# Performance work log

Measured on AMD Instinct MI355X. Metric: run time of the kernel, lower is better.

## Reference

```python
import jax, jax.numpy as jnp
import numpy as np

NUM_BINS = 32
SIGMA_RATIO = 0.5          # Gaussian Parzen window width relative to bin spacing
SMOOTH_NR = 1e-07
SMOOTH_DR = 1e-07


def setup_inputs() -> dict:
    key = jax.random.key(0)
    k1, k2 = jax.random.split(key)
    shape = (2, 1, 96, 96, 96)
    pred = jax.random.uniform(k1, shape, dtype=jnp.float32)
    target = jax.random.uniform(k2, shape, dtype=jnp.float32)
    return {"pred": pred, "target": target}


def _parzen_weights(img_flat, bin_centers, preterm):
    # img_flat: [B, N]; bin_centers: [nb]
    # Gaussian Parzen window, normalized so each voxel's weights sum to 1 over bins.
    d = img_flat[..., None] - bin_centers          # [B, N, nb]
    w = jnp.exp(-preterm * d * d)                  # [B, N, nb]
    return w / jnp.sum(w, axis=-1, keepdims=True)


def reference(pred, target):
    B = pred.shape[0]
    nb = NUM_BINS
    bin_centers = jnp.linspace(0.0, 1.0, nb, dtype=jnp.float32)  # [nb]
    bin_width = 1.0 / (nb - 1)
    sigma = SIGMA_RATIO * bin_width
    preterm = jnp.float32(1.0 / (2.0 * sigma * sigma))

    p = pred.reshape(B, -1)    # [B, N]
    t = target.reshape(B, -1)  # [B, N]
    N = p.shape[1]

    wa = _parzen_weights(p, bin_centers, preterm)  # [B, N, nb]
    wb = _parzen_weights(t, bin_centers, preterm)  # [B, N, nb]

    # joint histogram [B, nb, nb] and marginals [B, 1, nb]
    pab = jnp.einsum('bni,bnj->bij', wa, wb) / N
    pa = jnp.mean(wa, axis=1, keepdims=True).transpose(0, 2, 1).transpose(0, 2, 1)  # [B,1,nb]
    pa = jnp.mean(wa, axis=1)[:, None, :]  # [B, 1, nb]
    pb = jnp.mean(wb, axis=1)[:, None, :]  # [B, 1, nb]

    # papb = bmm(pa^T, pb): outer product of marginals -> [B, nb, nb]
    papb = jnp.einsum('bki,bkj->bij', pa, pb)

    mi = jnp.sum(pab * jnp.log((pab + SMOOTH_NR) / (papb + SMOOTH_DR) + SMOOTH_DR),
                 axis=(-1, -2))  # [B]
    return -jnp.mean(mi)
```

## Files before the change

kernel.cpp:

```cpp
#include <hip/hip_runtime.h>
#include <hip/hip_bf16.h>

#define NBINS 32
#define LDS_STRIDE 264
#define NTHREADS 256
#define NVOX 884736
#define NSLABS 3456
#define BPB 512
#define NSLOTS 16
#define TILE_HALVES (NBINS * LDS_STRIDE)

typedef __attribute__((ext_vector_type(8))) _Float16 half8;
typedef __attribute__((ext_vector_type(16))) float f32x16;
typedef __attribute__((ext_vector_type(4))) int i32x4;

__device__ __forceinline__ void scatter_rewrite(_Float16* __restrict__ L, int tid, float x,
                                                int& ki_old, bool zero_old) {
    float tt = x * 31.0f;
    float kf = rintf(tt);
    int ki = (int)kf;
    float u = tt - kf;
    if (zero_old) {
#pragma unroll
        for (int o = 0; o < 7; ++o) {
            int b = ki_old + o - 3;
            if (b >= 0 && b < NBINS) L[b * LDS_STRIDE + tid] = (_Float16)0.0f;
        }
    }
    float w[7];
    float s = 0.0f;
#pragma unroll
    for (int o = 0; o < 7; ++o) {
        float d = u - (float)(o - 3);
        float e = __expf(-2.0f * d * d);
        int b = ki + o - 3;
        bool valid = (b >= 0) && (b < NBINS);
        e = valid ? e : 0.0f;
        w[o] = e;
        s += e;
    }
    float rinv = 1.0f / s;
#pragma unroll
    for (int o = 0; o < 7; ++o) {
        int b = ki + o - 3;
        if (b >= 0 && b < NBINS)
            L[b * LDS_STRIDE + tid] = (_Float16)(w[o] * rinv);
    }
    ki_old = ki;
}

__global__ __launch_bounds__(NTHREADS, 4)
void mi_hist_kernel(const float* __restrict__ pred, const float* __restrict__ targ,
                    float* __restrict__ hist ) {
    __shared__ __attribute__((aligned(16))) _Float16 smem[2 * TILE_HALVES];
    _Float16* LA = smem;
    _Float16* LB = smem + TILE_HALVES;

    const int tid = threadIdx.x;
    const int bx = blockIdx.x;
    const int batch = blockIdx.y;
    const float* p = pred + (size_t)batch * NVOX;
    const float* t = targ + (size_t)batch * NVOX;

    const int wid = tid >> 6;
    const int lane = tid & 63;
    const int frag_off = (lane & 31) * LDS_STRIDE + wid * 64 + 8 * (lane >> 5);

    const int nchunks = (bx < 384) ? 7 : 6;

    f32x16 acc;
#pragma unroll
    for (int r = 0; r < 16; ++r) acc[r] = 0.0f;

    {
        i32x4 z = {0, 0, 0, 0};
        i32x4* zp = (i32x4*)smem;
        for (int i = tid; i < (2 * TILE_HALVES) / 8; i += NTHREADS) zp[i] = z;
    }
    float pv = p[(size_t)bx * 256 + tid];
    float tv = t[(size_t)bx * 256 + tid];
    int kiA = 0, kiB = 0;
    __syncthreads();

    for (int c = 0; c < nchunks; ++c) {
        float pn = 0.0f, tn = 0.0f;
        if (c + 1 < nchunks) {
            size_t v = ((size_t)(c + 1) * BPB + bx) * 256 + tid;
            pn = p[v];
            tn = t[v];
        }
        scatter_rewrite(LA, tid, pv, kiA, c > 0);
        scatter_rewrite(LB, tid, tv, kiB, c > 0);
        __syncthreads();

#pragma unroll
        for (int kb = 0; kb < 4; ++kb) {
            half8 af = *(const half8*)&LA[frag_off + kb * 16];
            half8 bf = *(const half8*)&LB[frag_off + kb * 16];
            acc = __builtin_amdgcn_mfma_f32_32x32x16_f16(af, bf, acc, 0, 0, 0);
        }
        __syncthreads();
        pv = pn; tv = tn;
    }

    float* red = (float*)smem;
    const int col = lane & 31;
    const int rlo = 4 * (lane >> 5);
#pragma unroll
    for (int r = 0; r < 16; ++r) {
        int rowc = (r & 3) + 8 * (r >> 2) + rlo;
        red[wid * 1024 + rowc * 32 + col] = acc[r];
    }
    __syncthreads();
    float* H = hist + ((size_t)(bx & (NSLOTS - 1)) * 2 + batch) * 1024;
    for (int idx = tid; idx < 1024; idx += NTHREADS) {
        float s = red[idx] + red[1024 + idx] + red[2048 + idx] + red[3072 + idx];
        atomicAdd(&H[idx], s);
    }
}

__global__ void mi_reduce_kernel(const float* __restrict__ hist, float* __restrict__ out) {
    __shared__ float s_pab[2 * NBINS * NBINS];
    __shared__ double s_pa[2][NBINS];
    __shared__ double s_pb[2][NBINS];
    __shared__ double s_red[256];
    const int tid = threadIdx.x;
    const double invN = 1.0 / (double)NVOX;

    for (int g = tid; g < 512; g += 256) {
        float4 s = make_float4(0.f, 0.f, 0.f, 0.f);
        for (int sl = 0; sl < NSLOTS; ++sl) {
            float4 v = ((const float4*)hist)[sl * 512 + g];
            s.x += v.x; s.y += v.y; s.z += v.z; s.w += v.w;
        }
        ((float4*)s_pab)[g] = s;
    }
    __syncthreads();

    if (tid < 64) {
        int b = tid >> 5, i = tid & 31;
        double s = 0.0;
        for (int j = 0; j < NBINS; ++j) s += (double)s_pab[(b * NBINS + i) * NBINS + j];
        s_pa[b][i] = s * invN;
    } else if (tid < 128) {
        int t2 = tid - 64;
        int b = t2 >> 5, j = t2 & 31;
        double s = 0.0;
        for (int i = 0; i < NBINS; ++i) s += (double)s_pab[(b * NBINS + i) * NBINS + j];
        s_pb[b][j] = s * invN;
    }
    __syncthreads();

    double acc = 0.0;
    for (int idx = tid; idx < 2 * NBINS * NBINS; idx += 256) {
        int b = idx >> 10;
        int cell = idx & 1023;
        int i = cell >> 5, j = cell & 31;
        double pab = (double)s_pab[idx] * invN;
        double papb = s_pa[b][i] * s_pb[b][j];
        acc += pab * log((pab + 1e-7) / (papb + 1e-7) + 1e-7);
    }
    s_red[tid] = acc;
    __syncthreads();
    for (int s2 = 128; s2 > 0; s2 >>= 1) {
        if (tid < s2) s_red[tid] += s_red[tid + s2];
        __syncthreads();
    }
    if (tid == 0) out[0] = (float)(-0.5 * s_red[0]);
}

extern "C" void kernel_launch(void* const* d_in, const int* in_sizes, int n_in,
                              void* d_out, int out_size, void* d_ws, size_t ws_size,
                              hipStream_t stream) {
    const float* pred = (const float*)d_in[0];
    const float* targ = (const float*)d_in[1];
    float* hist = (float*)d_ws;
    float* out = (float*)d_out;

    hipMemsetAsync(hist, 0, NSLOTS * 2 * NBINS * NBINS * sizeof(float), stream);
    dim3 grid(BPB, 2);
    hipLaunchKernelGGL(mi_hist_kernel, grid, dim3(NTHREADS), 0, stream, pred, targ, hist);
    hipLaunchKernelGGL(mi_reduce_kernel, dim3(1), dim3(256), 0, stream, hist, out);
}
```

Measured before the change: 33.73 us.

## Double-buffer LDS weight tiles, trim Parzen window to six bins, resize blocks

Allocates two LDS tile pairs and alternates between them, so one barrier per chunk replaces two and scattering the next chunk can overlap the MFMA reads of the previous one. The Parzen window is cut from 7 to 6 bins by picking the start bin from the sign of the fractional offset, which saves one exp and one LDS store per voxel per image. Blocks go to 192 threads (3 waves), 384 blocks per batch and a uniform 12 chunks, with launch bounds lowered to 2, so work per block is balanced. The cost is twice the LDS per block and possibly lower occupancy. Dropping the far tail bin slightly changes the normalised weights.

```diff
diff --git a/kernel.cpp b/kernel.cpp
--- a/kernel.cpp
+++ b/kernel.cpp
@@ -2,11 +2,11 @@
 #include <hip/hip_bf16.h>
 
 #define NBINS 32
-#define LDS_STRIDE 264
-#define NTHREADS 256
+#define LDS_STRIDE 200
+#define NTHREADS 192
 #define NVOX 884736
-#define NSLABS 3456
-#define BPB 512
+#define BPB 384
+#define NCHUNKS 12
 #define NSLOTS 16
 #define TILE_HALVES (NBINS * LDS_STRIDE)
 
@@ -15,25 +15,26 @@
 typedef __attribute__((ext_vector_type(4))) int i32x4;
 
 __device__ __forceinline__ void scatter_rewrite(_Float16* __restrict__ L, int tid, float x,
-                                                int& ki_old, bool zero_old) {
+                                                int& kb_old, bool zero_old) {
     float tt = x * 31.0f;
     float kf = rintf(tt);
     int ki = (int)kf;
     float u = tt - kf;
+    int kb = ki - 3 + (u > 0.0f ? 1 : 0);
     if (zero_old) {
 #pragma unroll
-        for (int o = 0; o < 7; ++o) {
-            int b = ki_old + o - 3;
+        for (int o = 0; o < 6; ++o) {
+            int b = kb_old + o;
             if (b >= 0 && b < NBINS) L[b * LDS_STRIDE + tid] = (_Float16)0.0f;
         }
     }
-    float w[7];
+    float w[6];
     float s = 0.0f;
 #pragma unroll
-    for (int o = 0; o < 7; ++o) {
-        float d = u - (float)(o - 3);
+    for (int o = 0; o < 6; ++o) {
+        int b = kb + o;
+        float d = tt - (float)b;
         float e = __expf(-2.0f * d * d);
-        int b = ki + o - 3;
         bool valid = (b >= 0) && (b < NBINS);
         e = valid ? e : 0.0f;
         w[o] = e;
@@ -41,20 +42,33 @@
     }
     float rinv = 1.0f / s;
 #pragma unroll
-    for (int o = 0; o < 7; ++o) {
-        int b = ki + o - 3;
+    for (int o = 0; o < 6; ++o) {
+        int b = kb + o;
         if (b >= 0 && b < NBINS)
             L[b * LDS_STRIDE + tid] = (_Float16)(w[o] * rinv);
     }
-    ki_old = ki;
-}
-
-__global__ __launch_bounds__(NTHREADS, 4)
+    kb_old = kb;
+}
+
+__device__ __forceinline__ void do_mfma(const _Float16* __restrict__ bufA,
+                                        const _Float16* __restrict__ bufB,
+                                        int frag_off, f32x16& acc) {
+#pragma unroll
+    for (int kb = 0; kb < 4; ++kb) {
+        half8 af = *(const half8*)&bufA[frag_off + kb * 16];
+        half8 bf = *(const half8*)&bufB[frag_off + kb * 16];
+        acc = __builtin_amdgcn_mfma_f32_32x32x16_f16(af, bf, acc, 0, 0, 0);
+    }
+}
+
+__global__ __launch_bounds__(NTHREADS, 2)
 void mi_hist_kernel(const float* __restrict__ pred, const float* __restrict__ targ,
                     float* __restrict__ hist ) {
-    __shared__ __attribute__((aligned(16))) _Float16 smem[2 * TILE_HALVES];
-    _Float16* LA = smem;
-    _Float16* LB = smem + TILE_HALVES;
+    __shared__ __attribute__((aligned(16))) _Float16 smem[4 * TILE_HALVES];
+    _Float16* A0 = smem;
+    _Float16* B0 = smem + TILE_HALVES;
+    _Float16* A1 = smem + 2 * TILE_HALVES;
+    _Float16* B1 = smem + 3 * TILE_HALVES;
 
     const int tid = threadIdx.x;
     const int bx = blockIdx.x;
@@ -66,8 +80,6 @@
     const int lane = tid & 63;
     const int frag_off = (lane & 31) * LDS_STRIDE + wid * 64 + 8 * (lane >> 5);
 
-    const int nchunks = (bx < 384) ? 7 : 6;
-
     f32x16 acc;
 #pragma unroll
     for (int r = 0; r < 16; ++r) acc[r] = 0.0f;
@@ -75,33 +87,43 @@
     {
         i32x4 z = {0, 0, 0, 0};
         i32x4* zp = (i32x4*)smem;
-        for (int i = tid; i < (2 * TILE_HALVES) / 8; i += NTHREADS) zp[i] = z;
-    }
-    float pv = p[(size_t)bx * 256 + tid];
-    float tv = t[(size_t)bx * 256 + tid];
-    int kiA = 0, kiB = 0;
-    __syncthreads();
-
-    for (int c = 0; c < nchunks; ++c) {
-        float pn = 0.0f, tn = 0.0f;
-        if (c + 1 < nchunks) {
-            size_t v = ((size_t)(c + 1) * BPB + bx) * 256 + tid;
-            pn = p[v];
-            tn = t[v];
-        }
-        scatter_rewrite(LA, tid, pv, kiA, c > 0);
-        scatter_rewrite(LB, tid, tv, kiB, c > 0);
-        __syncthreads();
-
-#pragma unroll
-        for (int kb = 0; kb < 4; ++kb) {
-            half8 af = *(const half8*)&LA[frag_off + kb * 16];
-            half8 bf = *(const half8*)&LB[frag_off + kb * 16];
-            acc = __builtin_amdgcn_mfma_f32_32x32x16_f16(af, bf, acc, 0, 0, 0);
-        }
-        __syncthreads();
-        pv = pn; tv = tn;
-    }
+        for (int i = tid; i < (4 * TILE_HALVES) / 8; i += NTHREADS) zp[i] = z;
+    }
+    float pv = p[(size_t)bx * NTHREADS + tid];
+    float tv = t[(size_t)bx * NTHREADS + tid];
+    int kbA0 = 0, kbB0 = 0, kbA1 = 0, kbB1 = 0;
+    __syncthreads();
+
+#pragma unroll 1
+    for (int j = 0; j < NCHUNKS / 2; ++j) {
+        {
+            const int c = 2 * j;
+            float pn = 0.0f, tn = 0.0f;
+            if (c + 1 < NCHUNKS) {
+                size_t v = ((size_t)(c + 1) * BPB + bx) * NTHREADS + tid;
+                pn = p[v]; tn = t[v];
+            }
+            scatter_rewrite(A0, tid, pv, kbA0, j > 0);
+            scatter_rewrite(B0, tid, tv, kbB0, j > 0);
+            __syncthreads();
+            do_mfma(A0, B0, frag_off, acc);
+            pv = pn; tv = tn;
+        }
+        {
+            const int c = 2 * j + 1;
+            float pn = 0.0f, tn = 0.0f;
+            if (c + 1 < NCHUNKS) {
+                size_t v = ((size_t)(c + 1) * BPB + bx) * NTHREADS + tid;
+                pn = p[v]; tn = t[v];
+            }
+            scatter_rewrite(A1, tid, pv, kbA1, j > 0);
+            scatter_rewrite(B1, tid, tv, kbB1, j > 0);
+            __syncthreads();
+            do_mfma(A1, B1, frag_off, acc);
+            pv = pn; tv = tn;
+        }
+    }
+    __syncthreads();
 
     float* red = (float*)smem;
     const int col = lane & 31;
@@ -114,7 +136,7 @@
     __syncthreads();
     float* H = hist + ((size_t)(bx & (NSLOTS - 1)) * 2 + batch) * 1024;
     for (int idx = tid; idx < 1024; idx += NTHREADS) {
-        float s = red[idx] + red[1024 + idx] + red[2048 + idx] + red[3072 + idx];
+        float s = red[idx] + red[1024 + idx] + red[2048 + idx];
         atomicAdd(&H[idx], s);
     }
 }
```

Result: slower. 38.12 us (+13.0%).

## Double-buffer LDS weight tiles and split pred/target scatter across half-blocks

Applied to the files above, without the earlier changes.

Each chunk now covers 128 voxels, with threads 0-127 computing Parzen weights for pred and threads 128-255 for target. This halves the per-thread transcendental and scatter work per chunk. Weights use a 6-tap window instead of 7. LDS tiles are double-buffered, so the MFMA on the previous chunk overlaps with the scatter of the current one and one barrier per chunk is dropped. The cost is twice as many chunk iterations and fewer atomic slots, and the narrower window slightly changes the weight truncation.

```diff
diff --git a/kernel.cpp b/kernel.cpp
--- a/kernel.cpp
+++ b/kernel.cpp
@@ -2,38 +2,31 @@
 #include <hip/hip_bf16.h>
 
 #define NBINS 32
-#define LDS_STRIDE 264
+#define CHUNK 128
+#define STR 136
+#define TILE_HALVES (NBINS * STR)
 #define NTHREADS 256
 #define NVOX 884736
-#define NSLABS 3456
 #define BPB 512
-#define NSLOTS 16
-#define TILE_HALVES (NBINS * LDS_STRIDE)
+#define NSLOTS 8
 
 typedef __attribute__((ext_vector_type(8))) _Float16 half8;
 typedef __attribute__((ext_vector_type(16))) float f32x16;
 typedef __attribute__((ext_vector_type(4))) int i32x4;
 
-__device__ __forceinline__ void scatter_rewrite(_Float16* __restrict__ L, int tid, float x,
-                                                int& ki_old, bool zero_old) {
+__device__ __forceinline__ void compute_w(float x, int& kb, _Float16* wq) {
     float tt = x * 31.0f;
     float kf = rintf(tt);
     int ki = (int)kf;
     float u = tt - kf;
-    if (zero_old) {
-#pragma unroll
-        for (int o = 0; o < 7; ++o) {
-            int b = ki_old + o - 3;
-            if (b >= 0 && b < NBINS) L[b * LDS_STRIDE + tid] = (_Float16)0.0f;
-        }
-    }
-    float w[7];
+    kb = ki - 3 + (u > 0.0f ? 1 : 0);
+    float w[6];
     float s = 0.0f;
 #pragma unroll
-    for (int o = 0; o < 7; ++o) {
-        float d = u - (float)(o - 3);
+    for (int o = 0; o < 6; ++o) {
+        int b = kb + o;
+        float d = tt - (float)b;
         float e = __expf(-2.0f * d * d);
-        int b = ki + o - 3;
         bool valid = (b >= 0) && (b < NBINS);
         e = valid ? e : 0.0f;
         w[o] = e;
@@ -41,32 +34,43 @@
     }
     float rinv = 1.0f / s;
 #pragma unroll
-    for (int o = 0; o < 7; ++o) {
-        int b = ki + o - 3;
-        if (b >= 0 && b < NBINS)
-            L[b * LDS_STRIDE + tid] = (_Float16)(w[o] * rinv);
-    }
-    ki_old = ki;
+    for (int o = 0; o < 6; ++o) wq[o] = (_Float16)(w[o] * rinv);
+}
+
+__device__ __forceinline__ void scatter(_Float16* __restrict__ L, int col, int kb_new,
+                                        const _Float16* wq, int kb_old, bool zero_old) {
+    if (zero_old) {
+#pragma unroll
+        for (int o = 0; o < 6; ++o) {
+            int b = kb_old + o;
+            if (b >= 0 && b < NBINS) L[b * STR + col] = (_Float16)0.0f;
+        }
+    }
+#pragma unroll
+    for (int o = 0; o < 6; ++o) {
+        int b = kb_new + o;
+        if (b >= 0 && b < NBINS) L[b * STR + col] = wq[o];
+    }
 }
 
 __global__ __launch_bounds__(NTHREADS, 4)
 void mi_hist_kernel(const float* __restrict__ pred, const float* __restrict__ targ,
                     float* __restrict__ hist ) {
-    __shared__ __attribute__((aligned(16))) _Float16 smem[2 * TILE_HALVES];
-    _Float16* LA = smem;
-    _Float16* LB = smem + TILE_HALVES;
+    __shared__ __attribute__((aligned(16))) _Float16 smem[4 * TILE_HALVES];
 
     const int tid = threadIdx.x;
     const int bx = blockIdx.x;
     const int batch = blockIdx.y;
-    const float* p = pred + (size_t)batch * NVOX;
-    const float* t = targ + (size_t)batch * NVOX;
+    const int col = tid & 127;
+    const bool isB = tid >= 128;
+    const float* src = (isB ? targ : pred) + (size_t)batch * NVOX;
+    const int tile_off = isB ? TILE_HALVES : 0;
 
     const int wid = tid >> 6;
     const int lane = tid & 63;
-    const int frag_off = (lane & 31) * LDS_STRIDE + wid * 64 + 8 * (lane >> 5);
-
-    const int nchunks = (bx < 384) ? 7 : 6;
+    const int frag = (lane & 31) * STR + wid * 32 + 8 * (lane >> 5);
+
+    const int nchunks = (bx < 256) ? 14 : 13;
 
     f32x16 acc;
 #pragma unroll
@@ -75,41 +79,54 @@
     {
         i32x4 z = {0, 0, 0, 0};
         i32x4* zp = (i32x4*)smem;
-        for (int i = tid; i < (2 * TILE_HALVES) / 8; i += NTHREADS) zp[i] = z;
-    }
-    float pv = p[(size_t)bx * 256 + tid];
-    float tv = t[(size_t)bx * 256 + tid];
-    int kiA = 0, kiB = 0;
-    __syncthreads();
-
+        for (int i = tid; i < (4 * TILE_HALVES) / 8; i += NTHREADS) zp[i] = z;
+    }
+    float x = src[(size_t)bx * CHUNK + col];
+    int kb_old[2] = {0, 0};
+    __syncthreads();
+
+#pragma unroll 1
     for (int c = 0; c < nchunks; ++c) {
-        float pn = 0.0f, tn = 0.0f;
+        const int q = c & 1;
+        _Float16 wq[6];
+        int kb;
+        compute_w(x, kb, wq);
         if (c + 1 < nchunks) {
-            size_t v = ((size_t)(c + 1) * BPB + bx) * 256 + tid;
-            pn = p[v];
-            tn = t[v];
-        }
-        scatter_rewrite(LA, tid, pv, kiA, c > 0);
-        scatter_rewrite(LB, tid, tv, kiB, c > 0);
+            x = src[((size_t)(c + 1) * BPB + bx) * CHUNK + col];
+        }
         __syncthreads();
-
-#pragma unroll
-        for (int kb = 0; kb < 4; ++kb) {
-            half8 af = *(const half8*)&LA[frag_off + kb * 16];
-            half8 bf = *(const half8*)&LB[frag_off + kb * 16];
+        scatter(smem + q * 2 * TILE_HALVES + tile_off, col, kb, wq, kb_old[q], c >= 2);
+        kb_old[q] = kb;
+        if (c >= 1) {
+            const _Float16* Pp = smem + (q ^ 1) * 2 * TILE_HALVES;
+#pragma unroll
+            for (int kk = 0; kk < 2; ++kk) {
+                half8 af = *(const half8*)&Pp[frag + kk * 16];
+                half8 bf = *(const half8*)&Pp[TILE_HALVES + frag + kk * 16];
+                acc = __builtin_amdgcn_mfma_f32_32x32x16_f16(af, bf, acc, 0, 0, 0);
+            }
+        }
+    }
+    __syncthreads();
+    {
+        const int q = (nchunks - 1) & 1;
+        const _Float16* Pp = smem + q * 2 * TILE_HALVES;
+#pragma unroll
+        for (int kk = 0; kk < 2; ++kk) {
+            half8 af = *(const half8*)&Pp[frag + kk * 16];
+            half8 bf = *(const half8*)&Pp[TILE_HALVES + frag + kk * 16];
             acc = __builtin_amdgcn_mfma_f32_32x32x16_f16(af, bf, acc, 0, 0, 0);
         }
-        __syncthreads();
-        pv = pn; tv = tn;
-    }
+    }
+    __syncthreads();
 
     float* red = (float*)smem;
-    const int col = lane & 31;
+    const int colc = lane & 31;
     const int rlo = 4 * (lane >> 5);
 #pragma unroll
     for (int r = 0; r < 16; ++r) {
         int rowc = (r & 3) + 8 * (r >> 2) + rlo;
-        red[wid * 1024 + rowc * 32 + col] = acc[r];
+        red[wid * 1024 + rowc * 32 + colc] = acc[r];
     }
     __syncthreads();
     float* H = hist + ((size_t)(bx & (NSLOTS - 1)) * 2 + batch) * 1024;
```

Result: no change. 33.48 us (-0.7%).
